# Optimization experiments

Measured on AMD Instinct MI355X. Metric: run time of the kernel, lower is better.

## Reference

```python
import jax, jax.numpy as jnp
import numpy as np

N_FFT = 512
HOP = 128
REF_MIC = 0
B, C, T = 8, 8, 64000


def hann(n):
    # periodic Hann, like torch.hann_window
    return 0.5 - 0.5 * jnp.cos(2.0 * jnp.pi * jnp.arange(n) / n)


def stft(x, n_fft, hop, window):
    # torch.stft with center=True, reflect padding, onesided
    pad = n_fft // 2
    pads = [(0, 0)] * (x.ndim - 1) + [(pad, pad)]
    xp = jnp.pad(x, pads, mode="reflect")
    n_frames = 1 + (xp.shape[-1] - n_fft) // hop
    idx = jnp.arange(n_frames)[:, None] * hop + jnp.arange(n_fft)[None, :]
    frames = xp[..., idx] * window                  # (..., N, n_fft)
    X = jnp.fft.rfft(frames, axis=-1)               # (..., N, F)
    return jnp.swapaxes(X, -1, -2)                  # (..., F, N)


def istft(X, n_fft, hop, window):
    # torch.istft: windowed overlap-add with squared-window normalization
    pad = n_fft // 2
    Xt = jnp.swapaxes(X, -1, -2)                    # (..., N, F)
    frames = jnp.fft.irfft(Xt, n=n_fft, axis=-1) * window  # (..., N, n_fft)
    n_frames = frames.shape[-2]
    out_len = n_fft + hop * (n_frames - 1)
    idx = jnp.arange(n_frames)[:, None] * hop + jnp.arange(n_fft)[None, :]
    y = jnp.zeros(frames.shape[:-2] + (out_len,), frames.dtype).at[..., idx].add(frames)
    wsum = jnp.zeros((out_len,), frames.dtype).at[idx].add(
        jnp.broadcast_to(window ** 2, (n_frames, n_fft)))
    y = y / jnp.maximum(wsum, 1e-10)
    return y[..., pad:out_len - pad]                # undo center padding


def mwf_forward(x, w1, b1, w2, b2):
    window = hann(N_FFT).astype(x.dtype)
    X = stft(x, N_FFT, HOP, window)                 # (B, C, F, N) complex
    X = X[..., 1:, :]                               # drop DC bin -> F' = n_fft//2
    b, c, fp, n = X.shape
    # --- mask model: 2-layer MLP on |X_ref| over frequency, per frame ---
    Xref = X[..., REF_MIC, :, :]                    # (B, F', N)
    feat = jnp.abs(Xref).swapaxes(-1, -2)           # (B, N, F')
    h = jax.nn.relu(feat @ w1 + b1)                 # (B, N, H)
    m = jax.nn.sigmoid(h @ w2 + b2)                 # (B, N, 2*F')
    masks = m.reshape(b, n, 2, fp).transpose(0, 2, 3, 1)[:, None]  # (B,1,2,F',N)
    mask_t = masks[..., 0, :, :]                    # (B, 1, F', N)
    mask_n = masks[..., 1, :, :]
    # --- masked spatial covariance matrices ---
    R_tgt = jnp.einsum("bsfn,bcfn,bdfn->bsfcd", mask_t, X, X.conj())
    R_noise = jnp.einsum("bsfn,bcfn,bdfn->bsfcd", mask_n, X, X.conj())
    # --- MWF beamforming weights: (R_t + R_n)^{-1} R_t e_ref ---
    rhs = R_tgt[..., REF_MIC]                       # (B, 1, F', C)
    bf = jnp.linalg.solve(R_tgt + R_noise, rhs[..., None])[..., 0]
    Xe = jnp.einsum("bcfn,bsfc->bsfn", X, bf.conj())  # (B, 1, F', N)
    # pad DC bin back with zeros
    Xe = jnp.concatenate([jnp.zeros(Xe.shape[:-2] + (1, n), Xe.dtype), Xe], axis=-2)
    y = istft(Xe, N_FFT, HOP, window)               # (B, 1, T')
    t = x.shape[-1]
    if y.shape[-1] < t:
        y = jnp.concatenate(
            [y, jnp.zeros(y.shape[:-1] + (t - y.shape[-1],), y.dtype)], axis=-1)
    else:
        y = y[..., :t]
    return y


def setup_inputs() -> dict:
    key = jax.random.key(0)
    k1, k2, k3 = jax.random.split(key, 3)
    fp, hid = N_FFT // 2, 512
    x = jax.random.normal(k1, (B, C, T), dtype=jnp.float32)
    w1 = jax.random.normal(k2, (fp, hid), dtype=jnp.float32) * (1.0 / np.sqrt(fp))
    b1 = jnp.zeros((hid,), dtype=jnp.float32)
    w2 = jax.random.normal(k3, (hid, 2 * fp), dtype=jnp.float32) * (1.0 / np.sqrt(hid))
    b2 = jnp.zeros((2 * fp,), dtype=jnp.float32)
    return {"x": x, "w1": w1, "b1": b1, "w2": w2, "b2": b2}


def reference(x, w1, b1, w2, b2):
    return mwf_forward(x, w1, b1, w2, b2)
```

## Files before the change

kernel.cpp:

```cpp
#include <hip/hip_runtime.h>
#include <hip/hip_bf16.h>
#include <math.h>

#define NFFT 512
#define HOP  128
#define PADW 256
#define TLEN 64000
#define NF   501
#define NFP  504
#define FP   256
#define CH   8
#define BATCH 8
#define HID  512
#define MROWS (BATCH * NF)
#define FPB  8
#define NGRP 63
#define NSTG 4

#define S2C 0.70710678118654752f

typedef short bf16x8 __attribute__((ext_vector_type(8)));
typedef float f32x4 __attribute__((ext_vector_type(4)));

__device__ __forceinline__ unsigned short f2bf(float v) {
    __hip_bfloat16 hb = __float2bfloat16(v);
    return *reinterpret_cast<unsigned short*>(&hb);
}
__device__ __forceinline__ float bf2f(unsigned short u) {
    unsigned int t = ((unsigned int)u) << 16;
    float f;
    __builtin_memcpy(&f, &t, 4);
    return f;
}
__device__ __forceinline__ float2 bf2c(ushort2 v) { return make_float2(bf2f(v.x), bf2f(v.y)); }
__device__ __forceinline__ ushort2 c2bf(float2 v) { ushort2 o; o.x = f2bf(v.x); o.y = f2bf(v.y); return o; }

__device__ __forceinline__ float2 cadd(float2 a, float2 b) { return make_float2(a.x + b.x, a.y + b.y); }
__device__ __forceinline__ float2 csub(float2 a, float2 b) { return make_float2(a.x - b.x, a.y - b.y); }
__device__ __forceinline__ float2 cmul(float2 a, float2 b) { return make_float2(a.x * b.x - a.y * b.y, a.x * b.y + a.y * b.x); }
__device__ __forceinline__ float2 mulnegi(float2 a) { return make_float2(a.y, -a.x); }

__device__ __forceinline__ void dft8(const float2 u[8], float2 v[8]) {
    float2 a0 = cadd(u[0], u[4]), a1 = cadd(u[1], u[5]), a2 = cadd(u[2], u[6]), a3 = cadd(u[3], u[7]);
    float2 b0 = csub(u[0], u[4]), b1 = csub(u[1], u[5]), b2 = csub(u[2], u[6]), b3 = csub(u[3], u[7]);
    float2 c0 = cadd(a0, a2), c1 = csub(a0, a2), c2 = cadd(a1, a3), c3 = csub(a1, a3);
    v[0] = cadd(c0, c2); v[4] = csub(c0, c2);
    float2 nic3 = mulnegi(c3);
    v[2] = cadd(c1, nic3); v[6] = csub(c1, nic3);
    float2 d1 = make_float2(S2C * (b1.x + b1.y), S2C * (b1.y - b1.x));
    float2 d2 = mulnegi(b2);
    float2 d3 = make_float2(S2C * (b3.y - b3.x), -S2C * (b3.x + b3.y));
    float2 e0 = cadd(b0, d2), e1 = csub(b0, d2), e2 = cadd(d1, d3), e3 = csub(d1, d3);
    v[1] = cadd(e0, e2); v[5] = csub(e0, e2);
    float2 nie3 = mulnegi(e3);
    v[3] = cadd(e1, nie3); v[7] = csub(e1, nie3);
}

__device__ __forceinline__ int refl(int j) {
    j = (j < 0) ? -j : j;
    j = (j >= TLEN) ? 2 * (TLEN - 1) - j : j;
    return j;
}

__global__ __launch_bounds__(256) void k_prep(const float* __restrict__ w1,
                                              const float* __restrict__ w2,
                                              float* __restrict__ tw,
                                              unsigned short* __restrict__ wt1,
                                              unsigned short* __restrict__ wt2) {
    __shared__ float tile[32][33];
    int bid = blockIdx.x;
    if (bid == 384) {
        #pragma unroll
        for (int r = 0; r < 2; ++r) {
            int e = threadIdx.x + 256 * r;
            float ang = (float)(2.0 * M_PI * (double)e / 512.0);
            tw[e] = 0.5f - 0.5f * cosf(ang);
        }
        return;
    }
    const float* w; unsigned short* wt; int K, lb;
    if (bid < 128) { w = w1; wt = wt1; K = 256; lb = bid; }
    else           { w = w2; wt = wt2; K = 512; lb = bid - 128; }
    int nt = lb & 15, kt = lb >> 4;
    int tx = threadIdx.x & 31, ty = threadIdx.x >> 5;
    #pragma unroll
    for (int r = 0; r < 4; ++r)
        tile[ty + 8 * r][tx] = w[(size_t)(kt * 32 + ty + 8 * r) * HID + nt * 32 + tx];
    __syncthreads();
    #pragma unroll
    for (int r = 0; r < 4; ++r)
        wt[(size_t)(nt * 32 + ty + 8 * r) * K + kt * 32 + tx] = f2bf(tile[tx][ty + 8 * r]);
}

#define A_S 580
#define B_S 544
__global__ __launch_bounds__(256, 4) void k_stft(const float* __restrict__ x,
                                                 const float* __restrict__ tw,
                                                 ushort2* __restrict__ X,
                                                 unsigned short* __restrict__ featbf) {
    __shared__ float2 Abuf[4 * A_S];
    __shared__ float2 Bbuf[4 * B_S];
    __shared__ float2 Twd[512];
    int blk = blockIdx.x;
    int g = blk % NGRP;
    int bc = blk / NGRP;
    int c = bc % CH, b = bc / CH;
    int m0 = g * FPB;
    int tid = threadIdx.x;
    const float* xp = x + (size_t)(b * CH + c) * TLEN;

    #pragma unroll
    for (int r = 0; r < 2; ++r) {
        int e = tid + 256 * r;
        float se, ce;
        sincosf((float)e * (float)(2.0 * M_PI / 512.0), &se, &ce);
        Twd[e] = make_float2(ce, -se);
    }

    float* xs = (float*)Bbuf;
    int base = m0 * HOP - PADW;
    #pragma unroll
    for (int r = 0; r < 6; ++r) {
        int i = r * 256 + tid;
        xs[i] = xp[refl(base + i)];
    }
    __syncthreads();

    #pragma unroll
    for (int r = 0; r < 8; ++r) {
        int flat = r * 256 + tid;
        int sig = flat >> 9, t = flat & 511;
        float w = tw[t];
        Abuf[sig * A_S + t] = make_float2(xs[2 * sig * 128 + t] * w,
                                          xs[(2 * sig + 1) * 128 + t] * w);
    }
    __syncthreads();

    int sig = tid >> 6, dft = tid & 63;
    float2 u[8], v[8];

    {
        const float2* Az = &Abuf[sig * A_S];
        float2* Bu = &Bbuf[sig * B_S];
        #pragma unroll
        for (int a = 0; a < 8; ++a) u[a] = Az[64 * a + dft];
        dft8(u, v);
        #pragma unroll
        for (int k0 = 0; k0 < 8; ++k0) Bu[k0 * 68 + dft] = v[k0];
    }
    __syncthreads();

    {
        int k0 = dft >> 3, cd = dft & 7;
        const float2* Bu = &Bbuf[sig * B_S];
        float2* Au = &Abuf[sig * A_S];
        #pragma unroll
        for (int bb = 0; bb < 8; ++bb) u[bb] = Bu[k0 * 68 + 8 * bb + cd];
        #pragma unroll
        for (int bb = 1; bb < 8; ++bb) u[bb] = cmul(u[bb], Twd[(8 * bb * k0) & 511]);
        dft8(u, v);
        #pragma unroll
        for (int k1 = 0; k1 < 8; ++k1) Au[(8 * k0 + k1) * 9 + cd] = v[k1];
    }
    __syncthreads();

    {
        int k0 = dft >> 3, k1 = dft & 7;
        int kk = k0 + 8 * k1;
        const float2* Au = &Abuf[sig * A_S];
        float2* Bz = &Bbuf[sig * B_S];
        #pragma unroll
        for (int cd = 0; cd < 8; ++cd) u[cd] = Au[dft * 9 + cd];
        #pragma unroll
        for (int cd = 1; cd < 8; ++cd) u[cd] = cmul(u[cd], Twd[(cd * kk) & 511]);
        dft8(u, v);
        #pragma unroll
        for (int k2 = 0; k2 < 8; ++k2) Bz[kk + 64 * k2] = v[k2];
    }
    __syncthreads();

    {
        int kp = tid;
        int k = kp + 1;
        #pragma unroll
        for (int s = 0; s < 4; ++s) {
            float2 z1 = Bbuf[s * B_S + k];
            float2 z2 = Bbuf[s * B_S + (512 - k)];
            float Ar = 0.5f * (z1.x + z2.x);
            float Ai = 0.5f * (z1.y - z2.y);
            float Br = 0.5f * (z1.y + z2.y);
            float Bi = 0.5f * (z2.x - z1.x);
            int ma = m0 + 2 * s, mb_ = ma + 1;
            if (ma < NF) {
                X[((size_t)(b * NF + ma) * CH + c) * FP + kp] = c2bf(make_float2(Ar, Ai));
                if (c == 0) featbf[((size_t)b * NF + ma) * FP + kp] = f2bf(sqrtf(Ar * Ar + Ai * Ai));
            }
            if (mb_ < NF) {
                X[((size_t)(b * NF + mb_) * CH + c) * FP + kp] = c2bf(make_float2(Br, Bi));
                if (c == 0) featbf[((size_t)b * NF + mb_) * FP + kp] = f2bf(sqrtf(Br * Br + Bi * Bi));
            }
        }
    }
}

template<int K, int ACT>
__global__ __launch_bounds__(256) void k_mfma_mlp(const unsigned short* __restrict__ Abf,
                                                  const unsigned short* __restrict__ Wt,
                                                  const float* __restrict__ bias,
                                                  unsigned short* __restrict__ outbf,
                                                  int M) {
    __shared__ unsigned short Al[64][40];
    __shared__ unsigned short Bl[128][40];
    int bid = blockIdx.x;
    int nt = bid & 3, mt = bid >> 2;
    int m0 = mt * 64, n0 = nt * 128;
    int tid = threadIdx.x;
    int wid = tid >> 6, lane = tid & 63;
    int wm = wid >> 1, wn = wid & 1;
    int lr = lane & 15, lk = (lane >> 4) * 8;

    f32x4 acc[2][4] = {};

    int arow = tid >> 2, ak = (tid & 3) * 8;
    for (int k0 = 0; k0 < K; k0 += 32) {
        int garow = m0 + arow; if (garow > M - 1) garow = M - 1;
        float4 av = *(const float4*)&Abf[(size_t)garow * K + k0 + ak];
        int s0 = tid, s1 = tid + 256;
        float4 bv0 = *(const float4*)&Wt[(size_t)(n0 + (s0 >> 2)) * K + k0 + (s0 & 3) * 8];
        float4 bv1 = *(const float4*)&Wt[(size_t)(n0 + (s1 >> 2)) * K + k0 + (s1 & 3) * 8];
        if (k0 > 0) __syncthreads();
        *(float4*)&Al[arow][ak] = av;
        *(float4*)&Bl[s0 >> 2][(s0 & 3) * 8] = bv0;
        *(float4*)&Bl[s1 >> 2][(s1 & 3) * 8] = bv1;
        __syncthreads();
        bf16x8 af[2], bfr[4];
        af[0] = *(const bf16x8*)&Al[wm * 32 + lr][lk];
        af[1] = *(const bf16x8*)&Al[wm * 32 + 16 + lr][lk];
        #pragma unroll
        for (int nf = 0; nf < 4; ++nf)
            bfr[nf] = *(const bf16x8*)&Bl[wn * 64 + nf * 16 + lr][lk];
        #pragma unroll
        for (int mf = 0; mf < 2; ++mf)
            #pragma unroll
            for (int nf = 0; nf < 4; ++nf)
                acc[mf][nf] = __builtin_amdgcn_mfma_f32_16x16x32_bf16(af[mf], bfr[nf], acc[mf][nf], 0, 0, 0);
    }

    int rbase = (lane >> 4) * 4;
    #pragma unroll
    for (int mf = 0; mf < 2; ++mf) {
        #pragma unroll
        for (int nf = 0; nf < 4; ++nf) {
            int n = n0 + wn * 64 + nf * 16 + lr;
            float bj = bias[n];
            #pragma unroll
            for (int r = 0; r < 4; ++r) {
                int m = m0 + wm * 32 + mf * 16 + rbase + r;
                if (m < M) {
                    float vv = acc[mf][nf][r] + bj;
                    float o = (ACT == 0) ? fmaxf(vv, 0.f) : 1.f / (1.f + expf(-vv));
                    outbf[(size_t)m * HID + n] = f2bf(o);
                }
            }
        }
    }
}

__global__ __launch_bounds__(512) void k_cov(const ushort2* __restrict__ X,
                                             const unsigned short* __restrict__ mo,
                                             float2* __restrict__ part, int cck) {
    int nc = blockIdx.x, ftile = blockIdx.y, b = blockIdx.z;
    int tid = threadIdx.x;
    int c = tid >> 6;
    int ft = tid & 63;
    int f = ftile * 64 + ft;
    int n0 = nc * cck;
    int n1 = n0 + cck; if (n1 > NF) n1 = NF;

    __shared__ float2 vbuf[2][NSTG][CH][64];

    float ar[8], ai[8];
    #pragma unroll
    for (int d = 0; d < 8; ++d) { ar[d] = 0.f; ai[d] = 0.f; }
    float rr = 0.f, ri = 0.f;

    const ushort2* Xb = X + (size_t)b * NF * CH * FP;
    const unsigned short* mb = mo + (size_t)b * NF * HID;

    #pragma unroll
    for (int r = 0; r < NSTG; ++r) {
        int n = n0 + r;
        if (n < n1) vbuf[0][r][c][ft] = bf2c(Xb[(size_t)(n * CH + c) * FP + f]);
    }
    __syncthreads();
    int cur = 0;
    for (int nb = n0; nb < n1; nb += NSTG) {
        int nbn = nb + NSTG;
        ushort2 nx[NSTG];
        #pragma unroll
        for (int r = 0; r < NSTG; ++r) {
            int n = nbn + r;
            if (n < n1) nx[r] = Xb[(size_t)(n * CH + c) * FP + f];
        }
        float mts[NSTG], mns[NSTG];
        #pragma unroll
        for (int r = 0; r < NSTG; ++r) {
            int n = nb + r;
            if (n < n1) {
                mts[r] = bf2f(mb[(size_t)n * HID + f]);
                mns[r] = bf2f(mb[(size_t)n * HID + FP + f]);
            }
        }
        #pragma unroll
        for (int r = 0; r < NSTG; ++r) {
            int n = nb + r;
            if (n < n1) {
                float mt = mts[r], mn = mns[r];
                float w = mt + mn;
                float2 xc = vbuf[cur][r][c][ft];
                #pragma unroll
                for (int d = 0; d < 8; ++d) {
                    float2 xd = vbuf[cur][r][d][ft];
                    float pr = xc.x * xd.x + xc.y * xd.y;
                    float pi = xc.y * xd.x - xc.x * xd.y;
                    ar[d] += w * pr; ai[d] += w * pi;
                    if (d == 0) { rr += mt * pr; ri += mt * pi; }
                }
            }
        }
        if (nbn < n1) {
            #pragma unroll
            for (int r = 0; r < NSTG; ++r) {
                int n = nbn + r;
                if (n < n1) vbuf[cur ^ 1][r][c][ft] = bf2c(nx[r]);
            }
        }
        __syncthreads();
        cur ^= 1;
    }
    float2* pp = part + (((size_t)nc * BATCH + b) * FP + f) * 72;
    #pragma unroll
    for (int d = 0; d < 8; ++d)
        pp[c * 8 + d] = make_float2(ar[d], ai[d]);
    pp[64 + c] = make_float2(rr, ri);
}

__global__ __launch_bounds__(512) void k_cov_solve2(const float2* __restrict__ part,
                                                    float2* __restrict__ wc, int ncnt) {
    int blk = blockIdx.x;
    int fg = blk & 31;
    int b = blk >> 5;
    int tid = threadIdx.x;
    int c = tid >> 6, d = (tid >> 3) & 7, fl = tid & 7;
    int f = fg * 8 + fl;
    float ar = 0.f, ai = 0.f, rr = 0.f, ri = 0.f;
    const float2* pb = part + ((size_t)b * FP + f) * 72;
    for (int nc = 0; nc < ncnt; ++nc) {
        const float2* p = pb + (size_t)nc * BATCH * FP * 72;
        float2 v = p[c * 8 + d];
        ar += v.x; ai += v.y;
        if (d == 0) { float2 u = p[64 + c]; rr += u.x; ri += u.y; }
    }
    __shared__ float2 Am[8][73];
    __shared__ float2 rh[8][8];
    __shared__ float2 sl[8][9];
    Am[fl][c * 9 + d] = make_float2(ar, ai);
    if (d == 0) rh[fl][c] = make_float2(rr, ri);
    __syncthreads();
    if (tid < 8) {
        int ln = tid;
        float2* A = Am[ln];
        float2* r = rh[ln];
        float2* sol = sl[ln];
        for (int kk = 0; kk < 8; ++kk) {
            float2 pp = A[kk * 9 + kk];
            float ip = 1.f / (pp.x * pp.x + pp.y * pp.y);
            float invr = pp.x * ip, invi = -pp.y * ip;
            for (int i = kk + 1; i < 8; ++i) {
                float2 aik = A[i * 9 + kk];
                float fr2 = aik.x * invr - aik.y * invi;
                float fi2 = aik.x * invi + aik.y * invr;
                for (int jj = kk; jj < 8; ++jj) {
                    float2 ak = A[kk * 9 + jj];
                    A[i * 9 + jj].x -= fr2 * ak.x - fi2 * ak.y;
                    A[i * 9 + jj].y -= fr2 * ak.y + fi2 * ak.x;
                }
                r[i].x -= fr2 * r[kk].x - fi2 * r[kk].y;
                r[i].y -= fr2 * r[kk].y + fi2 * r[kk].x;
            }
        }
        for (int kk = 7; kk >= 0; --kk) {
            float sr = r[kk].x, si = r[kk].y;
            for (int jj = kk + 1; jj < 8; ++jj) {
                float2 ak = A[kk * 9 + jj];
                float2 xj = sol[jj];
                sr -= ak.x * xj.x - ak.y * xj.y;
                si -= ak.x * xj.y + ak.y * xj.x;
            }
            float2 pp = A[kk * 9 + kk];
            float ip = 1.f / (pp.x * pp.x + pp.y * pp.y);
            sol[kk].x = (sr * pp.x + si * pp.y) * ip;
            sol[kk].y = (si * pp.x - sr * pp.y) * ip;
        }
        for (int cc = 0; cc < 8; ++cc)
            wc[((size_t)b * CH + cc) * FP + fg * 8 + ln] = make_float2(sol[cc].x, -sol[cc].y);
    }
}

__global__ __launch_bounds__(512) void k_istft_bf(const ushort2* __restrict__ X,
                                                  const float2* __restrict__ wc,
                                                  float* __restrict__ yfr) {
    __shared__ float2 Zp[4 * 512];
    __shared__ float2 Gl[16 * 32 * 5];
    int blk = blockIdx.x;
    int g = blk % NGRP, b = blk / NGRP;
    int m0 = g * FPB;
    int tid = threadIdx.x;

    if (tid < 4) Zp[tid * 512] = make_float2(0.f, 0.f);
    const ushort2* Xb0 = X + (size_t)b * NF * CH * FP;
    const float2* wcb = wc + (size_t)b * CH * FP;
    #pragma unroll
    for (int half = 0; half < 2; ++half) {
        int i = half * 512 + tid;
        int sig = i >> 8, kp = i & 255;
        int ma = m0 + 2 * sig, mb_ = ma + 1;
        float2 Xa = make_float2(0.f, 0.f), Xb = make_float2(0.f, 0.f);
        if (ma < NF) {
            #pragma unroll
            for (int c = 0; c < 8; ++c) {
                float2 xv = bf2c(Xb0[(size_t)(ma * CH + c) * FP + kp]);
                float2 wv = wcb[c * FP + kp];
                Xa.x += xv.x * wv.x - xv.y * wv.y;
                Xa.y += xv.x * wv.y + xv.y * wv.x;
            }
        }
        if (mb_ < NF) {
            #pragma unroll
            for (int c = 0; c < 8; ++c) {
                float2 xv = bf2c(Xb0[(size_t)(mb_ * CH + c) * FP + kp]);
                float2 wv = wcb[c * FP + kp];
                Xb.x += xv.x * wv.x - xv.y * wv.y;
                Xb.y += xv.x * wv.y + xv.y * wv.x;
            }
        }
        int k = kp + 1;
        if (k == 256) {
            Zp[sig * 512 + 256] = make_float2(Xa.x, Xb.x);
        } else {
            Zp[sig * 512 + k]       = make_float2(Xa.x - Xb.y, Xa.y + Xb.x);
            Zp[sig * 512 + 512 - k] = make_float2(Xa.x + Xb.y, Xb.x - Xa.y);
        }
    }
    __syncthreads();

    {
        int k1 = tid >> 5, tau = tid & 31;
        float sa, ca;
        sincosf((float)tau * (float)(2.0 * M_PI / 32.0), &sa, &ca);
        float stepc = ca, steps = sa;
        float gr[4], gi[4];
        #pragma unroll
        for (int s = 0; s < 4; ++s) { gr[s] = 0.f; gi[s] = 0.f; }
        float cr = 1.f, ci = 0.f;
        #pragma unroll 4
        for (int k2 = 0; k2 < 32; ++k2) {
            int k = k1 + 16 * k2;
            #pragma unroll
            for (int s = 0; s < 4; ++s) {
                float2 z = Zp[s * 512 + k];
                gr[s] += z.x * cr - z.y * ci;
                gi[s] += z.x * ci + z.y * cr;
            }
            float ncr = cr * stepc - ci * steps;
            ci = cr * steps + ci * stepc;
            cr = ncr;
        }
        #pragma unroll
        for (int s = 0; s < 4; ++s)
            Gl[(k1 * 32 + tau) * 5 + s] = make_float2(gr[s], gi[s]);
    }
    __syncthreads();

    int t = tid;
    int tau = t & 31;
    float sa2, ca2;
    sincosf((float)t * (float)(2.0 * M_PI / 512.0), &sa2, &ca2);
    float stepc = ca2, steps = sa2;
    float accr[4], acci[4];
    #pragma unroll
    for (int s = 0; s < 4; ++s) { accr[s] = 0.f; acci[s] = 0.f; }
    float cr = 1.f, ci = 0.f;
    #pragma unroll 4
    for (int k1 = 0; k1 < 16; ++k1) {
        #pragma unroll
        for (int s = 0; s < 4; ++s) {
            float2 gv = Gl[(k1 * 32 + tau) * 5 + s];
            accr[s] += gv.x * cr - gv.y * ci;
            acci[s] += gv.x * ci + gv.y * cr;
        }
        float ncr = cr * stepc - ci * steps;
        ci = cr * steps + ci * stepc;
        cr = ncr;
    }
    float wv = (0.5f - 0.5f * ca2) * (1.f / 512.f);
    #pragma unroll
    for (int s = 0; s < 4; ++s) {
        int ma = m0 + 2 * s, mb_ = ma + 1;
        if (ma < NF)  yfr[((size_t)b * NFP + ma) * 512 + t] = accr[s] * wv;
        if (mb_ < NF) yfr[((size_t)b * NFP + mb_) * 512 + t] = acci[s] * wv;
    }
}

__global__ __launch_bounds__(256) void k_out(const float* __restrict__ yfr,
                                             float* __restrict__ out) {
    int i = blockIdx.x * blockDim.x + threadIdx.x;
    if (i >= BATCH * TLEN) return;
    int b = i / TLEN;
    int t = i - b * TLEN;
    int p = t + PADW;
    int q = p & 127;
    int m0 = p >> 7;
    float sq, cq;
    sincosf((float)q * (float)(2.0 * M_PI / 512.0), &sq, &cq);
    float w4[4] = {0.5f - 0.5f * cq, 0.5f + 0.5f * sq, 0.5f + 0.5f * cq, 0.5f - 0.5f * sq};
    float val = 0.f, wsum = 0.f;
    const float* yb = yfr + (size_t)b * NFP * 512;
    #pragma unroll
    for (int dm = 0; dm < 4; ++dm) {
        int mm = m0 - dm;
        if (mm >= 0 && mm < NF) {
            val += yb[(size_t)mm * 512 + q + 128 * dm];
            wsum += w4[dm] * w4[dm];
        }
    }
    out[i] = val / fmaxf(wsum, 1e-10f);
}

extern "C" void kernel_launch(void* const* d_in, const int* in_sizes, int n_in,
                              void* d_out, int out_size, void* d_ws, size_t ws_size,
                              hipStream_t stream) {
    const float* x  = (const float*)d_in[0];
    const float* w1 = (const float*)d_in[1];
    const float* b1 = (const float*)d_in[2];
    const float* w2 = (const float*)d_in[3];
    const float* b2 = (const float*)d_in[4];

    float* ws = (float*)d_ws;
    size_t off = 0;
    float*  tw    = ws + off; off += 512;
    ushort2* X    = (ushort2*)(ws + off); off += (size_t)BATCH * NF * CH * FP;
    float2* wc    = (float2*)(ws + off); off += (size_t)BATCH * FP * CH * 2;
    float*  yfr   = ws + off; off += (size_t)BATCH * NFP * 512;
    unsigned short* featbf = (unsigned short*)(ws + off); off += (size_t)MROWS * FP / 2;
    unsigned short* hbf    = (unsigned short*)(ws + off); off += (size_t)MROWS * HID / 2;
    unsigned short* mobf   = (unsigned short*)(ws + off); off += (size_t)MROWS * HID / 2;
    unsigned short* wt1bf  = (unsigned short*)(ws + off); off += (size_t)HID * FP / 2;
    unsigned short* wt2bf  = (unsigned short*)(ws + off); off += (size_t)HID * HID / 2;
    float2* part  = (float2*)(ws + off);

    int cnck = 8, cck = 63;
    size_t need16 = (off + (size_t)16 * BATCH * FP * 72 * 4) * sizeof(float);
    if (ws_size >= need16) { cnck = 16; cck = 32; }

    k_prep<<<385, 256, 0, stream>>>(w1, w2, tw, wt1bf, wt2bf);
    k_stft<<<BATCH * CH * NGRP, 256, 0, stream>>>(x, tw, X, featbf);
    k_mfma_mlp<FP, 0><<<63 * 4, 256, 0, stream>>>(featbf, wt1bf, b1, hbf, MROWS);
    k_mfma_mlp<HID, 1><<<63 * 4, 256, 0, stream>>>(hbf, wt2bf, b2, mobf, MROWS);
    k_cov<<<dim3(cnck, 4, BATCH), 512, 0, stream>>>(X, mobf, part, cck);
    k_cov_solve2<<<BATCH * 32, 512, 0, stream>>>(part, wc, cnck);
    k_istft_bf<<<BATCH * NGRP, 512, 0, stream>>>(X, wc, yfr);
    k_out<<<(BATCH * TLEN + 255) / 256, 256, 0, stream>>>(yfr, (float*)d_out);
}
```

Measured before the change: 123.4 us.

## Fuse iSTFT overlap-add into inverse-DFT kernel and precompute twiddle table

Merges k_istft_bf and k_out into one kernel. Each block now computes 12 frames (with halo frames on both sides) and does the overlap-add and window normalization in shared memory, writing the final output directly. This removes the yfr intermediate buffer and one kernel launch. The prep kernel now stores a complex twiddle table that the STFT and iSTFT kernels load instead of calling sincos. Interior STFT blocks read their input with float4 loads and skip reflection indexing. The price is 50% more frames per iSTFT block, from recomputing halo frames, plus larger shared memory and register use.

New measurement: 127.1 us. +3.0%, slower.

```diff
diff --git a/kernel.cpp b/kernel.cpp
--- a/kernel.cpp
+++ b/kernel.cpp
@@ -7,7 +7,6 @@
 #define PADW 256
 #define TLEN 64000
 #define NF   501
-#define NFP  504
 #define FP   256
 #define CH   8
 #define BATCH 8
@@ -64,7 +63,7 @@
 
 __global__ __launch_bounds__(256) void k_prep(const float* __restrict__ w1,
                                               const float* __restrict__ w2,
-                                              float* __restrict__ tw,
+                                              float2* __restrict__ Twdg,
                                               unsigned short* __restrict__ wt1,
                                               unsigned short* __restrict__ wt2) {
     __shared__ float tile[32][33];
@@ -73,8 +72,9 @@
         #pragma unroll
         for (int r = 0; r < 2; ++r) {
             int e = threadIdx.x + 256 * r;
-            float ang = (float)(2.0 * M_PI * (double)e / 512.0);
-            tw[e] = 0.5f - 0.5f * cosf(ang);
+            float se, ce;
+            sincosf((float)e * (float)(2.0 * M_PI / 512.0), &se, &ce);
+            Twdg[e] = make_float2(ce, -se);
         }
         return;
     }
@@ -95,7 +95,7 @@
 #define A_S 580
 #define B_S 544
 __global__ __launch_bounds__(256, 4) void k_stft(const float* __restrict__ x,
-                                                 const float* __restrict__ tw,
+                                                 const float2* __restrict__ Twdg,
                                                  ushort2* __restrict__ X,
                                                  unsigned short* __restrict__ featbf) {
     __shared__ float2 Abuf[4 * A_S];
@@ -109,20 +109,22 @@
     int tid = threadIdx.x;
     const float* xp = x + (size_t)(b * CH + c) * TLEN;
 
-    #pragma unroll
-    for (int r = 0; r < 2; ++r) {
-        int e = tid + 256 * r;
-        float se, ce;
-        sincosf((float)e * (float)(2.0 * M_PI / 512.0), &se, &ce);
-        Twd[e] = make_float2(ce, -se);
-    }
+    Twd[tid] = Twdg[tid];
+    Twd[tid + 256] = Twdg[tid + 256];
 
     float* xs = (float*)Bbuf;
     int base = m0 * HOP - PADW;
-    #pragma unroll
-    for (int r = 0; r < 6; ++r) {
-        int i = r * 256 + tid;
-        xs[i] = xp[refl(base + i)];
+    if (g >= 1 && g <= 61) {
+        const float4* xv = (const float4*)(xp + base);
+        float4* xsv = (float4*)xs;
+        xsv[tid] = xv[tid];
+        if (tid < 128) xsv[tid + 256] = xv[tid + 256];
+    } else {
+        #pragma unroll
+        for (int r = 0; r < 6; ++r) {
+            int i = r * 256 + tid;
+            xs[i] = xp[refl(base + i)];
+        }
     }
     __syncthreads();
 
@@ -130,7 +132,7 @@
     for (int r = 0; r < 8; ++r) {
         int flat = r * 256 + tid;
         int sig = flat >> 9, t = flat & 511;
-        float w = tw[t];
+        float w = 0.5f - 0.5f * Twd[t].x;
         Abuf[sig * A_S + t] = make_float2(xs[2 * sig * 128 + t] * w,
                                           xs[(2 * sig + 1) * 128 + t] * w);
     }
@@ -407,26 +409,28 @@
     }
 }
 
-__global__ __launch_bounds__(512) void k_istft_bf(const ushort2* __restrict__ X,
-                                                  const float2* __restrict__ wc,
-                                                  float* __restrict__ yfr) {
-    __shared__ float2 Zp[4 * 512];
-    __shared__ float2 Gl[16 * 32 * 5];
+__global__ __launch_bounds__(512) void k_istft_out(const ushort2* __restrict__ X,
+                                                   const float2* __restrict__ wc,
+                                                   const float2* __restrict__ Twdg,
+                                                   float* __restrict__ out) {
+    __shared__ float2 Zp[6 * 512];
+    __shared__ float2 Gl[16 * 32 * 7];
     int blk = blockIdx.x;
     int g = blk % NGRP, b = blk / NGRP;
-    int m0 = g * FPB;
+    int P0 = 256 + g * 1024;
+    int mlo = 8 * g - 1;
     int tid = threadIdx.x;
 
-    if (tid < 4) Zp[tid * 512] = make_float2(0.f, 0.f);
+    if (tid < 6) Zp[tid * 512] = make_float2(0.f, 0.f);
     const ushort2* Xb0 = X + (size_t)b * NF * CH * FP;
     const float2* wcb = wc + (size_t)b * CH * FP;
     #pragma unroll
-    for (int half = 0; half < 2; ++half) {
-        int i = half * 512 + tid;
+    for (int it = 0; it < 3; ++it) {
+        int i = it * 512 + tid;
         int sig = i >> 8, kp = i & 255;
-        int ma = m0 + 2 * sig, mb_ = ma + 1;
+        int ma = mlo + 2 * sig, mb_ = ma + 1;
         float2 Xa = make_float2(0.f, 0.f), Xb = make_float2(0.f, 0.f);
-        if (ma < NF) {
+        if (ma >= 0 && ma < NF) {
             #pragma unroll
             for (int c = 0; c < 8; ++c) {
                 float2 xv = bf2c(Xb0[(size_t)(ma * CH + c) * FP + kp]);
@@ -435,7 +439,7 @@
                 Xa.y += xv.x * wv.y + xv.y * wv.x;
             }
         }
-        if (mb_ < NF) {
+        if (mb_ >= 0 && mb_ < NF) {
             #pragma unroll
             for (int c = 0; c < 8; ++c) {
                 float2 xv = bf2c(Xb0[(size_t)(mb_ * CH + c) * FP + kp]);
@@ -456,18 +460,17 @@
 
     {
         int k1 = tid >> 5, tau = tid & 31;
-        float sa, ca;
-        sincosf((float)tau * (float)(2.0 * M_PI / 32.0), &sa, &ca);
-        float stepc = ca, steps = sa;
-        float gr[4], gi[4];
-        #pragma unroll
-        for (int s = 0; s < 4; ++s) { gr[s] = 0.f; gi[s] = 0.f; }
+        float2 tw32 = Twdg[16 * tau];
+        float stepc = tw32.x, steps = -tw32.y;
+        float gr[6], gi[6];
+        #pragma unroll
+        for (int s = 0; s < 6; ++s) { gr[s] = 0.f; gi[s] = 0.f; }
         float cr = 1.f, ci = 0.f;
         #pragma unroll 4
         for (int k2 = 0; k2 < 32; ++k2) {
             int k = k1 + 16 * k2;
             #pragma unroll
-            for (int s = 0; s < 4; ++s) {
+            for (int s = 0; s < 6; ++s) {
                 float2 z = Zp[s * 512 + k];
                 gr[s] += z.x * cr - z.y * ci;
                 gi[s] += z.x * ci + z.y * cr;
@@ -477,64 +480,76 @@
             cr = ncr;
         }
         #pragma unroll
-        for (int s = 0; s < 4; ++s)
-            Gl[(k1 * 32 + tau) * 5 + s] = make_float2(gr[s], gi[s]);
+        for (int s = 0; s < 6; ++s)
+            Gl[(k1 * 32 + tau) * 7 + s] = make_float2(gr[s], gi[s]);
     }
     __syncthreads();
 
     int t = tid;
     int tau = t & 31;
-    float sa2, ca2;
-    sincosf((float)t * (float)(2.0 * M_PI / 512.0), &sa2, &ca2);
-    float stepc = ca2, steps = sa2;
-    float accr[4], acci[4];
-    #pragma unroll
-    for (int s = 0; s < 4; ++s) { accr[s] = 0.f; acci[s] = 0.f; }
-    float cr = 1.f, ci = 0.f;
-    #pragma unroll 4
-    for (int k1 = 0; k1 < 16; ++k1) {
-        #pragma unroll
-        for (int s = 0; s < 4; ++s) {
-            float2 gv = Gl[(k1 * 32 + tau) * 5 + s];
-            accr[s] += gv.x * cr - gv.y * ci;
-            acci[s] += gv.x * ci + gv.y * cr;
-        }
-        float ncr = cr * stepc - ci * steps;
-        ci = cr * steps + ci * stepc;
-        cr = ncr;
-    }
-    float wv = (0.5f - 0.5f * ca2) * (1.f / 512.f);
-    #pragma unroll
-    for (int s = 0; s < 4; ++s) {
-        int ma = m0 + 2 * s, mb_ = ma + 1;
-        if (ma < NF)  yfr[((size_t)b * NFP + ma) * 512 + t] = accr[s] * wv;
-        if (mb_ < NF) yfr[((size_t)b * NFP + mb_) * 512 + t] = acci[s] * wv;
-    }
-}
-
-__global__ __launch_bounds__(256) void k_out(const float* __restrict__ yfr,
-                                             float* __restrict__ out) {
-    int i = blockIdx.x * blockDim.x + threadIdx.x;
-    if (i >= BATCH * TLEN) return;
-    int b = i / TLEN;
-    int t = i - b * TLEN;
-    int p = t + PADW;
-    int q = p & 127;
-    int m0 = p >> 7;
-    float sq, cq;
-    sincosf((float)q * (float)(2.0 * M_PI / 512.0), &sq, &cq);
-    float w4[4] = {0.5f - 0.5f * cq, 0.5f + 0.5f * sq, 0.5f + 0.5f * cq, 0.5f - 0.5f * sq};
-    float val = 0.f, wsum = 0.f;
-    const float* yb = yfr + (size_t)b * NFP * 512;
-    #pragma unroll
-    for (int dm = 0; dm < 4; ++dm) {
-        int mm = m0 - dm;
-        if (mm >= 0 && mm < NF) {
-            val += yb[(size_t)mm * 512 + q + 128 * dm];
-            wsum += w4[dm] * w4[dm];
-        }
-    }
-    out[i] = val / fmaxf(wsum, 1e-10f);
+    float2 twt = Twdg[t];
+    float stepc = twt.x, steps = -twt.y;
+    float accr[6], acci[6];
+    #pragma unroll
+    for (int s = 0; s < 6; ++s) { accr[s] = 0.f; acci[s] = 0.f; }
+    {
+        float cr = 1.f, ci = 0.f;
+        #pragma unroll 4
+        for (int k1 = 0; k1 < 16; ++k1) {
+            #pragma unroll
+            for (int s = 0; s < 6; ++s) {
+                float2 gv = Gl[(k1 * 32 + tau) * 7 + s];
+                accr[s] += gv.x * cr - gv.y * ci;
+                acci[s] += gv.x * ci + gv.y * cr;
+            }
+            float ncr = cr * stepc - ci * steps;
+            ci = cr * steps + ci * stepc;
+            cr = ncr;
+        }
+    }
+    float wv = (0.5f - 0.5f * twt.x) * (1.f / 512.f);
+    #pragma unroll
+    for (int s = 0; s < 6; ++s) { accr[s] *= wv; acci[s] *= wv; }
+
+    float* ybuf = (float*)Zp;
+    __syncthreads();
+    ybuf[tid] = 0.f;
+    ybuf[tid + 512] = 0.f;
+    __syncthreads();
+    #pragma unroll
+    for (int ph = 0; ph < 4; ++ph) {
+        #pragma unroll
+        for (int j = 0; j < 3; ++j) {
+            int fo = ph + 4 * j;
+            int m = mlo + fo;
+            float val = (fo & 1) ? acci[fo >> 1] : accr[fo >> 1];
+            int idx = m * 128 + t - P0;
+            if (m >= 0 && m < NF && idx >= 0 && idx < 1024)
+                ybuf[idx] += val;
+        }
+        __syncthreads();
+    }
+
+    #pragma unroll
+    for (int r = 0; r < 2; ++r) {
+        int i = tid + 512 * r;
+        int p = P0 + i;
+        int tg = p - PADW;
+        if (tg < TLEN) {
+            int q = p & 127;
+            int m0p = p >> 7;
+            float2 twq = Twdg[q];
+            float cq = twq.x, sq = -twq.y;
+            float w4[4] = {0.5f - 0.5f * cq, 0.5f + 0.5f * sq, 0.5f + 0.5f * cq, 0.5f - 0.5f * sq};
+            float wsum = 0.f;
+            #pragma unroll
+            for (int dm = 0; dm < 4; ++dm) {
+                int mm = m0p - dm;
+                if (mm >= 0 && mm < NF) wsum += w4[dm] * w4[dm];
+            }
+            out[(size_t)b * TLEN + tg] = ybuf[i] / fmaxf(wsum, 1e-10f);
+        }
+    }
 }
 
 extern "C" void kernel_launch(void* const* d_in, const int* in_sizes, int n_in,
@@ -548,10 +563,9 @@
 
     float* ws = (float*)d_ws;
     size_t off = 0;
-    float*  tw    = ws + off; off += 512;
+    float2* Twdg  = (float2*)(ws + off); off += 1024;
     ushort2* X    = (ushort2*)(ws + off); off += (size_t)BATCH * NF * CH * FP;
     float2* wc    = (float2*)(ws + off); off += (size_t)BATCH * FP * CH * 2;
-    float*  yfr   = ws + off; off += (size_t)BATCH * NFP * 512;
     unsigned short* featbf = (unsigned short*)(ws + off); off += (size_t)MROWS * FP / 2;
     unsigned short* hbf    = (unsigned short*)(ws + off); off += (size_t)MROWS * HID / 2;
     unsigned short* mobf   = (unsigned short*)(ws + off); off += (size_t)MROWS * HID / 2;
@@ -563,12 +577,11 @@
     size_t need16 = (off + (size_t)16 * BATCH * FP * 72 * 4) * sizeof(float);
     if (ws_size >= need16) { cnck = 16; cck = 32; }
 
-    k_prep<<<385, 256, 0, stream>>>(w1, w2, tw, wt1bf, wt2bf);
-    k_stft<<<BATCH * CH * NGRP, 256, 0, stream>>>(x, tw, X, featbf);
+    k_prep<<<385, 256, 0, stream>>>(w1, w2, Twdg, wt1bf, wt2bf);
+    k_stft<<<BATCH * CH * NGRP, 256, 0, stream>>>(x, Twdg, X, featbf);
     k_mfma_mlp<FP, 0><<<63 * 4, 256, 0, stream>>>(featbf, wt1bf, b1, hbf, MROWS);
     k_mfma_mlp<HID, 1><<<63 * 4, 256, 0, stream>>>(hbf, wt2bf, b2, mobf, MROWS);
     k_cov<<<dim3(cnck, 4, BATCH), 512, 0, stream>>>(X, mobf, part, cck);
     k_cov_solve2<<<BATCH * 32, 512, 0, stream>>>(part, wc, cnck);
-    k_istft_bf<<<BATCH * NGRP, 512, 0, stream>>>(X, wc, yfr);
-    k_out<<<(BATCH * TLEN + 255) / 256, 256, 0, stream>>>(yfr, (float*)d_out);
-}
+    k_istft_out<<<BATCH * NGRP, 512, 0, stream>>>(X, wc, Twdg, (float*)d_out);
+}
```
